# Performance work log

Hardware: AMD Instinct MI355X
Metric: run time of the kernel (lower is better)

Reference implementation:

```python
import jax, jax.numpy as jnp
import numpy as np

B, T, N, F, CH = 64, 8, 2000, 16, 64  # batch, timesteps(=receptive field), nodes, in features, channels (h_dim//2)
TASK = CH          # task_dim = h_dim // 2
P_TREAT = 0.5      # args.p
P1 = 1.0           # args.p1
BN_EPS = 1e-5


def setup_inputs() -> dict:
    key = jax.random.key(0)
    ks = jax.random.split(key, 40)
    def rn(i, shape, s=0.1):
        return jax.random.normal(ks[i], shape, dtype=jnp.float32) * s
    return {
        "X": jax.random.normal(ks[0], (B, T, N, F), dtype=jnp.float32),
        "A": jax.random.uniform(ks[1], (N, N), dtype=jnp.float32),
        "C": jax.random.randint(ks[2], (B, N), 0, 2, dtype=jnp.int32),
        "Y": jax.random.uniform(ks[3], (B, N), dtype=jnp.float32),
        "Cc": jnp.zeros((B, N), jnp.float32),
        "start_w": rn(4, (CH, F)),
        "start_b": rn(5, (CH,), 0.01),
        "filt_w": rn(6, (3, CH, CH, 2)),
        "filt_b": rn(7, (3, CH), 0.01),
        "gate_w": rn(8, (3, CH, CH, 2)),
        "gate_b": rn(9, (3, CH), 0.01),
        "skip_w": rn(10, (3, CH, CH)),
        "skip_b": rn(11, (3, CH), 0.01),
        "bn_g": 1.0 + rn(12, (3, CH), 0.01),
        "bn_b": rn(13, (3, CH), 0.01),
        "nodevec1": jax.random.normal(ks[14], (N, 10), dtype=jnp.float32),
        "nodevec2": jax.random.normal(ks[15], (10, N), dtype=jnp.float32),
        "task_emb": rn(16, (TASK,)),
        "gcn_w": rn(17, (CH, 3 * CH)),
        "gcn_b": rn(18, (CH,), 0.01),
        "h0_w1": rn(19, (CH, TASK + CH)),
        "h0_b1": rn(20, (CH,), 0.01),
        "h0_w2": rn(21, (1, CH)),
        "h0_b2": rn(22, (1,), 0.01),
        "h1_w1": rn(23, (CH, TASK + CH)),
        "h1_b1": rn(24, (CH,), 0.01),
        "h1_w2": rn(25, (1, CH)),
        "h1_b2": rn(26, (1,), 0.01),
    }


def _conv1x1(x, w, b):
    # x: (B,Cin,N,L), w: (Cout,Cin)
    return jnp.einsum('bcnl,oc->bonl', x, w) + b[None, :, None, None]


def _dil_conv(x, w, b, d):
    # kernel (1,2), dilation d along time, no padding -> width shrinks by d
    L = x.shape[-1]
    y = (jnp.einsum('bcnl,oc->bonl', x[..., :L - d], w[:, :, 0])
         + jnp.einsum('bcnl,oc->bonl', x[..., d:], w[:, :, 1]))
    return y + b[None, :, None, None]


def reference(X, A, C, Y, Cc, start_w, start_b, filt_w, filt_b, gate_w, gate_b,
              skip_w, skip_b, bn_g, bn_b, nodevec1, nodevec2, task_emb, gcn_w, gcn_b,
              h0_w1, h0_b1, h0_w2, h0_b2, h1_w1, h1_b1, h1_w2, h1_b2):
    x = jnp.transpose(X, (0, 3, 2, 1))            # (B,F,N,T)
    x = _conv1x1(x, start_w, start_b)             # (B,CH,N,T)
    adp = jax.nn.softmax(jax.nn.relu(nodevec1 @ nodevec2), axis=1)  # (N,N)
    skip = None
    d = 1
    for i in range(3):  # layers, dilations 1,2,4
        res = x
        f = jnp.tanh(_dil_conv(res, filt_w[i], filt_b[i], d))
        g = jax.nn.sigmoid(_dil_conv(res, gate_w[i], gate_b[i], d))
        x = f * g
        s = _conv1x1(x, skip_w[i], skip_b[i])
        skip = s if skip is None else s + skip[..., -s.shape[-1]:]
        x = x + res[..., -x.shape[-1]:]
        # eval-mode BatchNorm2d with running_mean=0, running_var=1
        scale = (bn_g[i] / jnp.sqrt(1.0 + BN_EPS))[None, :, None, None]
        x = x * scale + bn_b[i][None, :, None, None]
        d *= 2
    # gcn on skip (width 1): out = [x, A@x, A@(A@x)] -> concat -> 1x1 (dropout=eval identity)
    x1 = jnp.einsum('bcvl,vw->bcwl', skip, adp)
    x2 = jnp.einsum('bcvl,vw->bcwl', x1, adp)
    h = jnp.concatenate([skip, x1, x2], axis=1)   # (B,3CH,N,1)
    gx = jax.nn.relu(_conv1x1(h, gcn_w, gcn_b))   # (B,CH,N,1)
    bs, _, n_nodes, _ = gx.shape
    task = jnp.broadcast_to(task_emb[None, :, None, None], (bs, TASK, n_nodes, 1))
    z = jnp.concatenate([task, gx], axis=1)       # (B,TASK+CH,N,1)

    def hyp(w1, b1, w2, b2):
        hh = jax.nn.relu(_conv1x1(z, w1, b1))
        return _conv1x1(hh, w2, b2).reshape(-1)

    y1 = jax.nn.sigmoid(hyp(h1_w1, h1_b1, h1_w2, h1_b2))
    y0 = jax.nn.sigmoid(hyp(h0_w1, h0_b1, h0_w2, h0_b2))
    t = C.reshape(-1)
    y = jnp.where(t > 0, y1, y0)
    yc = jnp.clip(y, 1e-7, 1.0 - 1e-7)
    Yf = Y.reshape(-1)
    bce = -jnp.mean(Yf * jnp.log(yc) + (1.0 - Yf) * jnp.log(1.0 - yc))
    # linear MMD (mmd2_lin, CFR): masked means, jit-friendly
    zb = jnp.transpose(z, (0, 2, 1, 3)).reshape(bs * n_nodes, -1)  # (B*N, TASK+CH)
    tm = (t > 0).astype(zb.dtype)
    mean_t = (tm @ zb) / jnp.maximum(tm.sum(), 1.0)
    mean_c = ((1.0 - tm) @ zb) / jnp.maximum((1.0 - tm).sum(), 1.0)
    imb = jnp.sum((2.0 * P_TREAT * mean_t - 2.0 * (1.0 - P_TREAT) * mean_c) ** 2)
    loss = bce + P1 * imb
    return (loss, y, y0, y1)
```

## Files before the change

kernel.cpp:

```cpp
#include <hip/hip_runtime.h>
#include <cstdint>

#define NB 64
#define TT 8
#define NN 2000
#define NF 16
#define NCH 64
#define NPAD 2048
#define BCD 4096
#define ITEMS 128000

#define OFF_ADPF  0
#define OFF_ST    4194304
#define OFF_X2    0
#define OFF_ADPT  8388608
#define OFF_S     10485760
#define OFF_X1F   18874368
#define OFF_X1T   27262976
#define OFF_C01   31457280
#define OFF_WGCNT (OFF_C01 + 128)
#define OFF_W1TT  (OFF_WGCNT + 12288)
#define OFF_PART  (OFF_W1TT + 8192)
#define OFF_RED   (OFF_PART + 270336)
#define OFF_WAW   (OFF_RED + 136)
#define OFF_SWW   (OFF_WAW + 24576)
#define OFF_WSTW  (OFF_SWW + 6144)

#define SWZK(k, x) (((k) & ~63) | (((((k) >> 3) & 7) ^ ((x) & 7)) << 3) | ((k) & 7))
#define GSWZ(n) ((((n) >> 3) ^ (n)) & 7)

typedef __attribute__((ext_vector_type(8))) short short8;
typedef __attribute__((ext_vector_type(4))) float f32x4;
typedef const __attribute__((address_space(1))) uint32_t* gas_t;
typedef __attribute__((address_space(3))) uint32_t* las_t;

__device__ __forceinline__ float fast_rcp(float x) { return __builtin_amdgcn_rcpf(x); }
__device__ __forceinline__ float fast_tanh(float x) {
    x = fminf(fmaxf(x, -10.f), 10.f);
    float e = __expf(2.f * x);
    return (e - 1.f) * fast_rcp(e + 1.f);
}
__device__ __forceinline__ float fast_sigmoid(float x) {
    return fast_rcp(1.f + __expf(-x));
}
__device__ __forceinline__ unsigned short f2bf(float f) {
    uint32_t u = __float_as_uint(f);
    u += 0x7fff + ((u >> 16) & 1);
    return (unsigned short)(u >> 16);
}
__device__ __forceinline__ float bf2f(unsigned short b) {
    return __uint_as_float(((uint32_t)b) << 16);
}

__global__ __launch_bounds__(256) void prep_kernel(const float* __restrict__ gcn_w,
                            const float* __restrict__ h0_w1, const float* __restrict__ h0_b1,
                            const float* __restrict__ h1_w1, const float* __restrict__ h1_b1,
                            const float* __restrict__ task_emb,
                            const float* __restrict__ filt_w, const float* __restrict__ gate_w,
                            const float* __restrict__ skip_w, const float* __restrict__ start_w,
                            float* __restrict__ c01, float* __restrict__ wgcnT,
                            float* __restrict__ w1tT,
                            unsigned short* __restrict__ waw,
                            unsigned short* __restrict__ sww,
                            unsigned short* __restrict__ wstw)
{
    const int GS = 64 * 256;
    int gt = blockIdx.x * 256 + threadIdx.x;
    for (int idx = gt; idx < 64 * 192; idx += GS) {
        int o = idx / 192, j = idx % 192;
        wgcnT[j * 64 + o] = gcn_w[idx];
    }
    for (int idx = gt; idx < 4096; idx += GS) {
        int o = idx >> 6, c = idx & 63;
        w1tT[c * 64 + o]        = h0_w1[o * 128 + 64 + c];
        w1tT[4096 + c * 64 + o] = h1_w1[o * 128 + 64 + c];
    }
    for (int job = gt; job < 3 * 128 * 16; job += GS) {
        int L = job / 2048, rem = job % 2048;
        int r = rem >> 4, chp = rem & 15;
        int cho = chp ^ (r & 15);
        #pragma unroll
        for (int i = 0; i < 8; ++i) {
            int k = cho * 8 + i, tap = k >> 6, c = k & 63;
            float v = (r < 64) ? filt_w[L * 8192 + r * 128 + c * 2 + tap]
                               : gate_w[L * 8192 + (r - 64) * 128 + c * 2 + tap];
            waw[((L * 128 + r) * 16 + chp) * 8 + i] = f2bf(v);
        }
    }
    for (int job = gt; job < 3 * 64 * 8; job += GS) {
        int L = job / 512, rem = job % 512;
        int o = rem >> 3, chp = rem & 7;
        int cho = chp ^ (o & 7);
        #pragma unroll
        for (int i = 0; i < 8; ++i)
            sww[((L * 64 + o) * 8 + chp) * 8 + i] = f2bf(skip_w[L * 4096 + o * 64 + cho * 8 + i]);
    }
    for (int job = gt; job < 64 * 16; job += GS) {
        int o = job >> 4, chp = job & 15;
        int cho = chp ^ (o & 15);
        #pragma unroll
        for (int i = 0; i < 8; ++i) {
            int k = cho * 8 + i;
            wstw[(o * 16 + chp) * 8 + i] = (k < 16) ? f2bf(start_w[o * 16 + k]) : (unsigned short)0;
        }
    }
    if (gt < 128) {
        int head = gt >> 6, o = gt & 63;
        const float* w1 = head ? h1_w1 : h0_w1;
        const float* b1 = head ? h1_b1 : h0_b1;
        float a = b1[o];
        for (int k = 0; k < 64; ++k) a = fmaf(w1[o * 128 + k], task_emb[k], a);
        c01[gt] = a;
    }
}

__global__ __launch_bounds__(256) void adp_kernel(const float* __restrict__ nv1,
                                                  const float* __restrict__ nv2,
                                                  float* __restrict__ adpF)
{
    __shared__ float nv1s[10];
    __shared__ float rbuf[4];
    int tid = threadIdx.x;
    int r = blockIdx.x;
    if (tid < 10) nv1s[tid] = nv1[r * 10 + tid];
    __syncthreads();

    float val[8];
    float vmax = -3.4e38f;
    #pragma unroll
    for (int s = 0; s < 8; ++s) {
        int j = tid + s * 256;
        if (j < NN) {
            float v = 0.f;
            #pragma unroll
            for (int k = 0; k < 10; ++k) v = fmaf(nv1s[k], nv2[k * NN + j], v);
            v = fmaxf(v, 0.f);
            val[s] = v;
            vmax = fmaxf(vmax, v);
        } else val[s] = -3.4e38f;
    }
    for (int off = 32; off; off >>= 1) vmax = fmaxf(vmax, __shfl_down(vmax, off, 64));
    if ((tid & 63) == 0) rbuf[tid >> 6] = vmax;
    __syncthreads();
    vmax = fmaxf(fmaxf(rbuf[0], rbuf[1]), fmaxf(rbuf[2], rbuf[3]));
    __syncthreads();
    float sum = 0.f;
    #pragma unroll
    for (int s = 0; s < 8; ++s) {
        int j = tid + s * 256;
        if (j < NN) { val[s] = expf(val[s] - vmax); sum += val[s]; }
    }
    for (int off = 32; off; off >>= 1) sum += __shfl_down(sum, off, 64);
    if ((tid & 63) == 0) rbuf[tid >> 6] = sum;
    __syncthreads();
    sum = rbuf[0] + rbuf[1] + rbuf[2] + rbuf[3];
    float inv = 1.f / sum;
    #pragma unroll
    for (int s = 0; s < 8; ++s) {
        int j = tid + s * 256;
        if (j < NN) adpF[(size_t)r * NPAD + j] = val[s] * inv;
    }
}

__global__ __launch_bounds__(256) void transpose_adp(const float* __restrict__ adpF,
                                                     unsigned short* __restrict__ adpT)
{
    __shared__ float tile[64][65];
    int tid = threadIdx.x;
    int r0 = blockIdx.x * 64;
    int j0 = blockIdx.y * 64;
    #pragma unroll
    for (int s = 0; s < 16; ++s) {
        int idx = s * 256 + tid;
        int i = idx >> 6, jj = idx & 63;
        int r = r0 + i, j = j0 + jj;
        tile[i][jj] = (r < NN && j < NN) ? adpF[(size_t)r * NPAD + j] : 0.f;
    }
    __syncthreads();
    #pragma unroll
    for (int s = 0; s < 2; ++s) {
        int slot = s * 256 + tid;
        int j = slot >> 3, ch = slot & 7;
        short8 v;
        #pragma unroll
        for (int e = 0; e < 8; ++e) v[e] = (short)f2bf(tile[ch * 8 + e][j]);
        *(short8*)&adpT[(size_t)(j0 + j) * NPAD + r0 + ((ch ^ (j & 7)) << 3)] = v;
    }
}

template<int NG, int WOUT>
__device__ __forceinline__ void mfma_phaseB(int L,
    const unsigned short* __restrict__ xb, unsigned short* __restrict__ gbuf,
    const unsigned short* __restrict__ WA, const float* __restrict__ biasAll,
    int wave, int lr, int lk)
{
    if (wave >= NG) return;
    int idx = wave * 16 + lr;
    int n = (idx / WOUT) * 8 + (idx % WOUT);
    f32x4 aF[4], aG[4];
    #pragma unroll
    for (int mt = 0; mt < 4; ++mt) {
        aF[mt] = (f32x4){0.f, 0.f, 0.f, 0.f};
        aG[mt] = (f32x4){0.f, 0.f, 0.f, 0.f};
    }
    #pragma unroll
    for (int ks = 0; ks < 4; ++ks) {
        short8 bv = *(const short8*)&xb[(n * 16 + ((ks * 4 + lk) ^ (n & 15))) * 8];
        #pragma unroll
        for (int mt = 0; mt < 4; ++mt) {
            int r = mt * 16 + lr;
            short8 av = *(const short8*)&WA[(r * 16 + ((ks * 4 + lk) ^ (r & 15))) * 8];
            aF[mt] = __builtin_amdgcn_mfma_f32_16x16x32_bf16(av, bv, aF[mt], 0, 0, 0);
        }
        #pragma unroll
        for (int mt = 0; mt < 4; ++mt) {
            int r = (mt + 4) * 16 + lr;
            short8 av = *(const short8*)&WA[(r * 16 + ((ks * 4 + lk) ^ (r & 15))) * 8];
            aG[mt] = __builtin_amdgcn_mfma_f32_16x16x32_bf16(av, bv, aG[mt], 0, 0, 0);
        }
    }
    int gs = GSWZ(n);
    #pragma unroll
    for (int mt = 0; mt < 4; ++mt) {
        int ob = mt * 16 + lk * 4;
        ushort4 p;
        p.x = f2bf(fast_tanh(aF[mt][0] + biasAll[L * 128 + ob + 0]) * fast_sigmoid(aG[mt][0] + biasAll[L * 128 + 64 + ob + 0]));
        p.y = f2bf(fast_tanh(aF[mt][1] + biasAll[L * 128 + ob + 1]) * fast_sigmoid(aG[mt][1] + biasAll[L * 128 + 64 + ob + 1]));
        p.z = f2bf(fast_tanh(aF[mt][2] + biasAll[L * 128 + ob + 2]) * fast_sigmoid(aG[mt][2] + biasAll[L * 128 + 64 + ob + 2]));
        p.w = f2bf(fast_tanh(aF[mt][3] + biasAll[L * 128 + ob + 3]) * fast_sigmoid(aG[mt][3] + biasAll[L * 128 + 64 + ob + 3]));
        *(ushort4*)&gbuf[((n * 8) + ((mt * 2 + (lk >> 1)) ^ gs)) * 8 + (lk & 1) * 4] = p;
    }
}

template<int L, int D, int WOUT, int DN>
__device__ __forceinline__ void phaseC_conv(unsigned short* __restrict__ xb,
    const unsigned short* __restrict__ gbuf,
    const float* __restrict__ bn_g, const float* __restrict__ bn_b,
    float xreg[2][8], int wave, int o)
{
    const int WOUT_NEXT = WOUT - DN;
    float bsc = bn_g[L * 64 + o] * rsqrtf(1.0f + 1e-5f);
    float bsh = bn_b[L * 64 + o];
    #pragma unroll
    for (int gi = 0; gi < 2; ++gi) {
        int g = wave * 2 + gi;
        #pragma unroll
        for (int t = 0; t < WOUT; ++t) {
            int n = g * 8 + t;
            float gv = bf2f(gbuf[(n * 8 + ((o >> 3) ^ GSWZ(n))) * 8 + (o & 7)]);
            float nx = (gv + xreg[gi][t + D]) * bsc + bsh;
            xreg[gi][t] = nx;
            unsigned short bfv = f2bf(nx);
            if (t < WOUT_NEXT)
                xb[(n * 16 + ((o >> 3) ^ (n & 15))) * 8 + (o & 7)] = bfv;
            if (t >= DN) {
                int n1 = n - DN;
                xb[(n1 * 16 + (((o >> 3) + 8) ^ (n1 & 15))) * 8 + (o & 7)] = bfv;
            }
        }
    }
}

__device__ __forceinline__ void phaseC_skip(int L, int LASTT,
    const unsigned short* __restrict__ gbuf, const unsigned short* __restrict__ SW,
    f32x4 skacc[4], int wave, int lr, int lk)
{
    if (wave >= 2) return;
    int g = wave * 16 + lr;
    int n = g * 8 + LASTT;
    int gs = GSWZ(n);
    #pragma unroll
    for (int ks = 0; ks < 2; ++ks) {
        short8 bv = *(const short8*)&gbuf[(n * 8 + ((ks * 4 + lk) ^ gs)) * 8];
        #pragma unroll
        for (int mt = 0; mt < 4; ++mt) {
            int r = mt * 16 + lr;
            short8 av = *(const short8*)&SW[((L * 64 + r) * 8 + ((ks * 4 + lk) ^ (r & 7))) * 8];
            skacc[mt] = __builtin_amdgcn_mfma_f32_16x16x32_bf16(av, bv, skacc[mt], 0, 0, 0);
        }
    }
}

__global__ __launch_bounds__(1024) void temporal_kernel(
    const float* __restrict__ X,
    const float* __restrict__ start_b,
    const unsigned short* __restrict__ waw,
    const unsigned short* __restrict__ sww,
    const unsigned short* __restrict__ wstw,
    const float* __restrict__ filt_b, const float* __restrict__ gate_b,
    const float* __restrict__ skip_b,
    const float* __restrict__ bn_g, const float* __restrict__ bn_b,
    float* __restrict__ S, unsigned short* __restrict__ St)
{
    extern __shared__ float smem[];
    unsigned short* xb   = (unsigned short*)smem;
    unsigned short* gbuf = (unsigned short*)(smem + 16384);
    unsigned short* WA   = (unsigned short*)(smem + 24576);
    unsigned short* SW   = (unsigned short*)(smem + 32768);
    float* biasAll       = smem + 38912;

    int tid = threadIdx.x;
    int wave = tid >> 6, lane = tid & 63;
    int lr = lane & 15, lk = lane >> 4;
    int o = lane;
    int item0 = blockIdx.x * 32;

    __builtin_amdgcn_global_load_lds((gas_t)(wstw + tid * 8), (las_t)(WA + tid * 8), 16, 0, 0);
    for (int idx = tid; idx < 1536; idx += 1024)
        __builtin_amdgcn_global_load_lds((gas_t)(sww + idx * 8), (las_t)(SW + idx * 8), 16, 0, 0);
    if (tid < 384) {
        int L = tid >> 7, oo = tid & 127;
        biasAll[tid] = (oo < 64) ? filt_b[L * 64 + oo] : gate_b[L * 64 + oo - 64];
    }
    {
        int n = tid >> 2, c = tid & 3;
        int g = n >> 3, t = n & 7;
        int ig = item0 + g, b = ig / NN, nn = ig - b * NN;
        short8 v = {0, 0, 0, 0, 0, 0, 0, 0};
        if (c < 2) {
            const float* src = &X[((size_t)(b * TT + t) * NN + nn) * NF + c * 8];
            float4 f0 = *(const float4*)src;
            float4 f1 = *(const float4*)(src + 4);
            v[0] = (short)f2bf(f0.x); v[1] = (short)f2bf(f0.y);
            v[2] = (short)f2bf(f0.z); v[3] = (short)f2bf(f0.w);
            v[4] = (short)f2bf(f1.x); v[5] = (short)f2bf(f1.y);
            v[6] = (short)f2bf(f1.z); v[7] = (short)f2bf(f1.w);
        }
        *(short8*)&xb[(n * 16 + (c ^ (n & 15))) * 8] = v;
    }
    __syncthreads();

    {
        f32x4 aS[4];
        #pragma unroll
        for (int mt = 0; mt < 4; ++mt) aS[mt] = (f32x4){0.f, 0.f, 0.f, 0.f};
        int n = wave * 16 + lr;
        short8 bv = *(const short8*)&xb[(n * 16 + (lk ^ (n & 15))) * 8];
        #pragma unroll
        for (int mt = 0; mt < 4; ++mt) {
            int r = mt * 16 + lr;
            short8 av = *(const short8*)&WA[(r * 16 + (lk ^ (r & 15))) * 8];
            aS[mt] = __builtin_amdgcn_mfma_f32_16x16x32_bf16(av, bv, aS[mt], 0, 0, 0);
        }
        int gs = GSWZ(n);
        #pragma unroll
        for (int mt = 0; mt < 4; ++mt) {
            ushort4 p;
            p.x = f2bf(aS[mt][0]); p.y = f2bf(aS[mt][1]);
            p.z = f2bf(aS[mt][2]); p.w = f2bf(aS[mt][3]);
            *(ushort4*)&gbuf[((n * 8) + ((mt * 2 + (lk >> 1)) ^ gs)) * 8 + (lk & 1) * 4] = p;
        }
    }
    __syncthreads();

    float xreg[2][8];
    f32x4 skacc[4];
    #pragma unroll
    for (int mt = 0; mt < 4; ++mt) skacc[mt] = (f32x4){0.f, 0.f, 0.f, 0.f};

    {
        __builtin_amdgcn_global_load_lds((gas_t)(waw + (size_t)tid * 8),
                                         (las_t)(WA + tid * 8), 16, 0, 0);
        __builtin_amdgcn_global_load_lds((gas_t)(waw + (size_t)(tid + 1024) * 8),
                                         (las_t)(WA + (tid + 1024) * 8), 16, 0, 0);
        float sb = start_b[o];
        #pragma unroll
        for (int gi = 0; gi < 2; ++gi) {
            int g = wave * 2 + gi;
            #pragma unroll
            for (int t = 0; t < 8; ++t) {
                int n = g * 8 + t;
                float gv = bf2f(gbuf[(n * 8 + ((o >> 3) ^ GSWZ(n))) * 8 + (o & 7)]) + sb;
                xreg[gi][t] = gv;
                unsigned short bfv = f2bf(gv);
                if (t < 7)
                    xb[(n * 16 + ((o >> 3) ^ (n & 15))) * 8 + (o & 7)] = bfv;
                if (t >= 1) {
                    int n1 = n - 1;
                    xb[(n1 * 16 + (((o >> 3) + 8) ^ (n1 & 15))) * 8 + (o & 7)] = bfv;
                }
            }
        }
    }
    __syncthreads();

    mfma_phaseB<14, 7>(0, xb, gbuf, WA, biasAll, wave, lr, lk);
    __syncthreads();
    phaseC_skip(0, 6, gbuf, SW, skacc, wave, lr, lk);
    phaseC_conv<0, 1, 7, 2>(xb, gbuf, bn_g, bn_b, xreg, wave, o);
    __builtin_amdgcn_global_load_lds((gas_t)(waw + (size_t)(2048 + tid) * 8),
                                     (las_t)(WA + tid * 8), 16, 0, 0);
    __builtin_amdgcn_global_load_lds((gas_t)(waw + (size_t)(2048 + tid + 1024) * 8),
                                     (las_t)(WA + (tid + 1024) * 8), 16, 0, 0);
    __syncthreads();

    mfma_phaseB<10, 5>(1, xb, gbuf, WA, biasAll, wave, lr, lk);
    __syncthreads();
    phaseC_skip(1, 4, gbuf, SW, skacc, wave, lr, lk);
    phaseC_conv<1, 2, 5, 4>(xb, gbuf, bn_g, bn_b, xreg, wave, o);
    __builtin_amdgcn_global_load_lds((gas_t)(waw + (size_t)(4096 + tid) * 8),
                                     (las_t)(WA + tid * 8), 16, 0, 0);
    __builtin_amdgcn_global_load_lds((gas_t)(waw + (size_t)(4096 + tid + 1024) * 8),
                                     (las_t)(WA + (tid + 1024) * 8), 16, 0, 0);
    __syncthreads();

    mfma_phaseB<2, 1>(2, xb, gbuf, WA, biasAll, wave, lr, lk);
    __syncthreads();
    phaseC_skip(2, 0, gbuf, SW, skacc, wave, lr, lk);

    if (wave < 2) {
        int g = wave * 16 + lr;
        int ig = item0 + g, b = ig / NN, nn = ig - b * NN;
        #pragma unroll
        for (int mt = 0; mt < 4; ++mt) {
            #pragma unroll
            for (int j = 0; j < 4; ++j) {
                int oo = mt * 16 + lk * 4 + j;
                float v = skacc[mt][j] + skip_b[oo] + skip_b[64 + oo] + skip_b[128 + oo];
                int bc = b * 64 + oo;
                S[(size_t)nn * BCD + bc] = v;
                St[(size_t)bc * NPAD + SWZK(nn, oo)] = f2bf(v);
            }
        }
    }
}

__global__ __launch_bounds__(256) void gemm_mfma(
    const unsigned short* __restrict__ A, const unsigned short* __restrict__ B,
    float* __restrict__ Cf, unsigned short* __restrict__ Ct)
{
    __shared__ unsigned short As[128 * 64];
    __shared__ unsigned short Bs[128 * 64];
    int tid = threadIdx.x;
    int wave = tid >> 6, lane = tid & 63;
    int lk = lane >> 4, lr = lane & 15;
    int n0 = blockIdx.x * 128, m0 = blockIdx.y * 128;
    int wm = wave >> 1, wn = wave & 1;

    f32x4 acc[4][4];
    #pragma unroll
    for (int i = 0; i < 4; ++i)
        #pragma unroll
        for (int j = 0; j < 4; ++j)
            acc[i][j] = (f32x4){0.f, 0.f, 0.f, 0.f};

    for (int k0 = 0; k0 < NPAD; k0 += 64) {
        #pragma unroll
        for (int i = 0; i < 4; ++i) {
            int chunk = wave * 4 + i;
            int row = chunk * 8 + (lane >> 3);
            int koff = (lane & 7) * 8;
            __builtin_amdgcn_global_load_lds(
                (gas_t)(A + (size_t)(m0 + row) * NPAD + k0 + koff),
                (las_t)(&As[chunk * 512]), 16, 0, 0);
            __builtin_amdgcn_global_load_lds(
                (gas_t)(B + (size_t)(n0 + row) * NPAD + k0 + koff),
                (las_t)(&Bs[chunk * 512]), 16, 0, 0);
        }
        __syncthreads();
        #pragma unroll
        for (int s = 0; s < 2; ++s) {
            short8 av[4], bv[4];
            #pragma unroll
            for (int f = 0; f < 4; ++f) {
                int m = wm * 64 + f * 16 + lr;
                int ca = ((s * 4 + lk) ^ (m & 7));
                av[f] = *(const short8*)&As[m * 64 + ca * 8];
                int n = wn * 64 + f * 16 + lr;
                int cb = ((s * 4 + lk) ^ (n & 7));
                bv[f] = *(const short8*)&Bs[n * 64 + cb * 8];
            }
            #pragma unroll
            for (int fi = 0; fi < 4; ++fi)
                #pragma unroll
                for (int fj = 0; fj < 4; ++fj)
                    acc[fi][fj] = __builtin_amdgcn_mfma_f32_16x16x32_bf16(
                        av[fi], bv[fj], acc[fi][fj], 0, 0, 0);
        }
        __syncthreads();
    }

    #pragma unroll
    for (int fi = 0; fi < 4; ++fi) {
        #pragma unroll
        for (int fj = 0; fj < 4; ++fj) {
            int m = m0 + wm * 64 + fi * 16 + lk * 4;
            int n = n0 + wn * 64 + fj * 16 + lr;
            f32x4 v = acc[fi][fj];
            if (Cf) {
                Cf[(size_t)(m + 0) * BCD + n] = v[0];
                Cf[(size_t)(m + 1) * BCD + n] = v[1];
                Cf[(size_t)(m + 2) * BCD + n] = v[2];
                Cf[(size_t)(m + 3) * BCD + n] = v[3];
            }
            if (Ct) {
                ushort4 p;
                p.x = f2bf(v[0]); p.y = f2bf(v[1]);
                p.z = f2bf(v[2]); p.w = f2bf(v[3]);
                *(ushort4*)&Ct[(size_t)n * NPAD + SWZK(m, n)] = p;
            }
        }
    }
}

__global__ __launch_bounds__(256) void head_kernel(
    const float* __restrict__ S, const float* __restrict__ x1f,
    const float* __restrict__ x2,
    const float* __restrict__ wgcnT, const float* __restrict__ gcn_b,
    const float* __restrict__ c01, const float* __restrict__ w1tT,
    const float* __restrict__ h0_w2, const float* __restrict__ h0_b2,
    const float* __restrict__ h1_w2, const float* __restrict__ h1_b2,
    const int* __restrict__ Ct, const float* __restrict__ Yf,
    float* __restrict__ out, float* __restrict__ partials)
{
    __shared__ float hl[4][4][192];
    __shared__ float gxl[4][4][64];
    int tid = threadIdx.x;
    int wave = tid >> 6, o = tid & 63;
    int wid = blockIdx.x * 4 + wave;
    float w2a = h0_w2[o], w2b = h1_w2[o];
    float b20 = h0_b2[0], b21 = h1_b2[0];
    float cb = gcn_b[o], c0a = c01[o], c0b = c01[64 + o];

    float accT = 0.f, accC = 0.f, bce = 0.f, cT = 0.f, cC = 0.f;

    for (int base = wid * 4; base < ITEMS; base += 2048 * 4) {
        #pragma unroll
        for (int it = 0; it < 4; ++it) {
            int item = base + it;
            int b = item / NN, n = item - b * NN;
            int bc = b * 64 + o;
            hl[wave][it][o]       = S[(size_t)n * BCD + bc];
            hl[wave][it][64 + o]  = x1f[(size_t)n * BCD + bc];
            hl[wave][it][128 + o] = x2[(size_t)n * BCD + bc];
        }
        float a0 = cb, a1 = cb, a2 = cb, a3 = cb;
        for (int j = 0; j < 192; ++j) {
            float w = wgcnT[j * 64 + o];
            a0 = fmaf(w, hl[wave][0][j], a0);
            a1 = fmaf(w, hl[wave][1][j], a1);
            a2 = fmaf(w, hl[wave][2][j], a2);
            a3 = fmaf(w, hl[wave][3][j], a3);
        }
        float gxv[4] = {fmaxf(a0, 0.f), fmaxf(a1, 0.f), fmaxf(a2, 0.f), fmaxf(a3, 0.f)};
        #pragma unroll
        for (int it = 0; it < 4; ++it) gxl[wave][it][o] = gxv[it];

        float p0[4], p1[4];
        #pragma unroll
        for (int it = 0; it < 4; ++it) { p0[it] = c0a; p1[it] = c0b; }
        for (int c = 0; c < 64; ++c) {
            float w0 = w1tT[c * 64 + o];
            float w1 = w1tT[4096 + c * 64 + o];
            float g0 = gxl[wave][0][c], g1 = gxl[wave][1][c];
            float g2 = gxl[wave][2][c], g3 = gxl[wave][3][c];
            p0[0] = fmaf(w0, g0, p0[0]); p0[1] = fmaf(w0, g1, p0[1]);
            p0[2] = fmaf(w0, g2, p0[2]); p0[3] = fmaf(w0, g3, p0[3]);
            p1[0] = fmaf(w1, g0, p1[0]); p1[1] = fmaf(w1, g1, p1[1]);
            p1[2] = fmaf(w1, g2, p1[2]); p1[3] = fmaf(w1, g3, p1[3]);
        }
        #pragma unroll
        for (int it = 0; it < 4; ++it) {
            float r0 = w2a * fmaxf(p0[it], 0.f);
            float r1 = w2b * fmaxf(p1[it], 0.f);
            #pragma unroll
            for (int off = 32; off; off >>= 1) {
                r0 += __shfl_down(r0, off, 64);
                r1 += __shfl_down(r1, off, 64);
            }
            int item = base + it;
            int tt = Ct[item];
            if (o == 0) {
                float y0 = 1.f / (1.f + expf(-(r0 + b20)));
                float y1 = 1.f / (1.f + expf(-(r1 + b21)));
                float y = (tt > 0) ? y1 : y0;
                out[1 + item] = y;
                out[1 + ITEMS + item] = y0;
                out[1 + 2 * ITEMS + item] = y1;
                float yc = fminf(fmaxf(y, 1e-7f), 1.f - 1e-7f);
                float Yv = Yf[item];
                bce -= Yv * logf(yc) + (1.f - Yv) * logf(1.f - yc);
                if (tt > 0) cT += 1.f; else cC += 1.f;
            }
            if (tt > 0) accT += gxv[it]; else accC += gxv[it];
        }
    }
    partials[wid * 132 + o] = accT;
    partials[wid * 132 + 64 + o] = accC;
    if (o == 0) {
        partials[wid * 132 + 128] = bce;
        partials[wid * 132 + 129] = cT;
        partials[wid * 132 + 130] = cC;
    }
}

__global__ __launch_bounds__(256) void reduce_kernel(const float* __restrict__ partials,
                                                     float* __restrict__ red)
{
    __shared__ float rb[4];
    int slot = blockIdx.x;
    int tid = threadIdx.x;
    float s = 0.f;
    for (int w = tid; w < 2048; w += 256) s += partials[w * 132 + slot];
    #pragma unroll
    for (int off = 32; off; off >>= 1) s += __shfl_down(s, off, 64);
    if ((tid & 63) == 0) rb[tid >> 6] = s;
    __syncthreads();
    if (tid == 0) red[slot] = rb[0] + rb[1] + rb[2] + rb[3];
}

__global__ void final_kernel(const float* __restrict__ red,
                             const float* __restrict__ task_emb,
                             float* __restrict__ out)
{
    int tid = threadIdx.x;
    float cT = red[129], cC = red[130];
    float iT = 1.f / fmaxf(cT, 1.f), iC = 1.f / fmaxf(cC, 1.f);
    float d1 = task_emb[tid] * (cT * iT) - task_emb[tid] * (cC * iC);
    float d2 = red[tid] * iT - red[64 + tid] * iC;
    float p = d1 * d1 + d2 * d2;
    #pragma unroll
    for (int off = 32; off; off >>= 1) p += __shfl_down(p, off, 64);
    if (tid == 0) out[0] = red[128] * (1.f / (float)ITEMS) + p;
}

extern "C" void kernel_launch(void* const* d_in, const int* in_sizes, int n_in,
                              void* d_out, int out_size, void* d_ws, size_t ws_size,
                              hipStream_t stream)
{
    const float* X       = (const float*)d_in[0];
    const int*   Ct      = (const int*)d_in[2];
    const float* Yf      = (const float*)d_in[3];
    const float* start_w = (const float*)d_in[5];
    const float* start_b = (const float*)d_in[6];
    const float* filt_w  = (const float*)d_in[7];
    const float* filt_b  = (const float*)d_in[8];
    const float* gate_w  = (const float*)d_in[9];
    const float* gate_b  = (const float*)d_in[10];
    const float* skip_w  = (const float*)d_in[11];
    const float* skip_b  = (const float*)d_in[12];
    const float* bn_g    = (const float*)d_in[13];
    const float* bn_b    = (const float*)d_in[14];
    const float* nv1     = (const float*)d_in[15];
    const float* nv2     = (const float*)d_in[16];
    const float* task    = (const float*)d_in[17];
    const float* gcn_w   = (const float*)d_in[18];
    const float* gcn_b   = (const float*)d_in[19];
    const float* h0_w1   = (const float*)d_in[20];
    const float* h0_b1   = (const float*)d_in[21];
    const float* h0_w2   = (const float*)d_in[22];
    const float* h0_b2   = (const float*)d_in[23];
    const float* h1_w1   = (const float*)d_in[24];
    const float* h1_b1   = (const float*)d_in[25];
    const float* h1_w2   = (const float*)d_in[26];
    const float* h1_b2   = (const float*)d_in[27];

    float* ws    = (float*)d_ws;
    float* adpF  = ws + OFF_ADPF;
    unsigned short* St   = (unsigned short*)(ws + OFF_ST);
    float* x2    = ws + OFF_X2;
    unsigned short* adpT = (unsigned short*)(ws + OFF_ADPT);
    float* S     = ws + OFF_S;
    float* x1f   = ws + OFF_X1F;
    unsigned short* x1t  = (unsigned short*)(ws + OFF_X1T);
    float* c01   = ws + OFF_C01;
    float* wgcnT = ws + OFF_WGCNT;
    float* w1tT  = ws + OFF_W1TT;
    float* part  = ws + OFF_PART;
    float* red   = ws + OFF_RED;
    unsigned short* waw  = (unsigned short*)(ws + OFF_WAW);
    unsigned short* sww  = (unsigned short*)(ws + OFF_SWW);
    unsigned short* wstw = (unsigned short*)(ws + OFF_WSTW);
    float* outp  = (float*)d_out;

    hipMemsetAsync(St, 0, (size_t)BCD * NPAD * sizeof(unsigned short), stream);

    prep_kernel<<<64, 256, 0, stream>>>(gcn_w, h0_w1, h0_b1, h1_w1, h1_b1, task,
                                        filt_w, gate_w, skip_w, start_w,
                                        c01, wgcnT, w1tT, waw, sww, wstw);
    adp_kernel<<<NN, 256, 0, stream>>>(nv1, nv2, adpF);
    dim3 tg(NPAD / 64, NPAD / 64);
    transpose_adp<<<tg, 256, 0, stream>>>(adpF, adpT);

    const int K2_LDS = 39296 * 4;
    hipFuncSetAttribute(reinterpret_cast<const void*>(temporal_kernel),
                        hipFuncAttributeMaxDynamicSharedMemorySize, K2_LDS);
    temporal_kernel<<<ITEMS / 32, 1024, K2_LDS, stream>>>(
        X, start_b, waw, sww, wstw, filt_b, gate_b,
        skip_b, bn_g, bn_b, S, St);

    dim3 gg(BCD / 128, NPAD / 128);
    gemm_mfma<<<gg, 256, 0, stream>>>(adpT, St, x1f, x1t);
    gemm_mfma<<<gg, 256, 0, stream>>>(adpT, x1t, x2, nullptr);

    head_kernel<<<512, 256, 0, stream>>>(S, x1f, x2, wgcnT, gcn_b, c01, w1tT,
                                         h0_w2, h0_b2, h1_w2, h1_b2,
                                         Ct, Yf, outp, part);
    reduce_kernel<<<131, 256, 0, stream>>>(part, red);
    final_kernel<<<1, 64, 0, stream>>>(red, task, outp);
}
```

Baseline: 530.3 us.

## Split dilated conv taps into two K=64 MFMA passes, halve temporal block items

```diff
diff --git a/kernel.cpp b/kernel.cpp
--- a/kernel.cpp
+++ b/kernel.cpp
@@ -75,33 +75,34 @@
         w1tT[c * 64 + o]        = h0_w1[o * 128 + 64 + c];
         w1tT[4096 + c * 64 + o] = h1_w1[o * 128 + 64 + c];
     }
-    for (int job = gt; job < 3 * 128 * 16; job += GS) {
+    for (int job = gt; job < 3 * 2 * 128 * 8; job += GS) {
         int L = job / 2048, rem = job % 2048;
-        int r = rem >> 4, chp = rem & 15;
-        int cho = chp ^ (r & 15);
+        int p = rem >> 10, rem2 = rem & 1023;
+        int r = rem2 >> 3, chp = rem2 & 7;
+        int cho = chp ^ (r & 7);
         #pragma unroll
         for (int i = 0; i < 8; ++i) {
-            int k = cho * 8 + i, tap = k >> 6, c = k & 63;
-            float v = (r < 64) ? filt_w[L * 8192 + r * 128 + c * 2 + tap]
-                               : gate_w[L * 8192 + (r - 64) * 128 + c * 2 + tap];
-            waw[((L * 128 + r) * 16 + chp) * 8 + i] = f2bf(v);
+            int c = cho * 8 + i;
+            float v = (r < 64) ? filt_w[L * 8192 + r * 128 + c * 2 + p]
+                               : gate_w[L * 8192 + (r - 64) * 128 + c * 2 + p];
+            waw[((L * 2 + p) * 128 + r) * 64 + chp * 8 + i] = f2bf(v);
         }
     }
     for (int job = gt; job < 3 * 64 * 8; job += GS) {
         int L = job / 512, rem = job % 512;
-        int o = rem >> 3, chp = rem & 7;
-        int cho = chp ^ (o & 7);
+        int r = rem >> 3, chp = rem & 7;
+        int cho = chp ^ (r & 7);
         #pragma unroll
         for (int i = 0; i < 8; ++i)
-            sww[((L * 64 + o) * 8 + chp) * 8 + i] = f2bf(skip_w[L * 4096 + o * 64 + cho * 8 + i]);
-    }
-    for (int job = gt; job < 64 * 16; job += GS) {
-        int o = job >> 4, chp = job & 15;
-        int cho = chp ^ (o & 15);
+            sww[(L * 64 + r) * 64 + chp * 8 + i] = f2bf(skip_w[L * 4096 + r * 64 + cho * 8 + i]);
+    }
+    for (int job = gt; job < 64 * 8; job += GS) {
+        int r = job >> 3, chp = job & 7;
+        int cho = chp ^ (r & 7);
         #pragma unroll
         for (int i = 0; i < 8; ++i) {
             int k = cho * 8 + i;
-            wstw[(o * 16 + chp) * 8 + i] = (k < 16) ? f2bf(start_w[o * 16 + k]) : (unsigned short)0;
+            wstw[r * 64 + chp * 8 + i] = (k < 16) ? f2bf(start_w[r * 16 + k]) : (unsigned short)0;
         }
     }
     if (gt < 128) {
@@ -188,7 +189,7 @@
     }
 }
 
-template<int NG, int WOUT>
+template<int NG, int WOUT, int D>
 __device__ __forceinline__ void mfma_phaseB(int L,
     const unsigned short* __restrict__ xb, unsigned short* __restrict__ gbuf,
     const unsigned short* __restrict__ WA, const float* __restrict__ biasAll,
@@ -204,19 +205,24 @@
         aG[mt] = (f32x4){0.f, 0.f, 0.f, 0.f};
     }
     #pragma unroll
-    for (int ks = 0; ks < 4; ++ks) {
-        short8 bv = *(const short8*)&xb[(n * 16 + ((ks * 4 + lk) ^ (n & 15))) * 8];
-        #pragma unroll
-        for (int mt = 0; mt < 4; ++mt) {
-            int r = mt * 16 + lr;
-            short8 av = *(const short8*)&WA[(r * 16 + ((ks * 4 + lk) ^ (r & 15))) * 8];
-            aF[mt] = __builtin_amdgcn_mfma_f32_16x16x32_bf16(av, bv, aF[mt], 0, 0, 0);
-        }
-        #pragma unroll
-        for (int mt = 0; mt < 4; ++mt) {
-            int r = (mt + 4) * 16 + lr;
-            short8 av = *(const short8*)&WA[(r * 16 + ((ks * 4 + lk) ^ (r & 15))) * 8];
-            aG[mt] = __builtin_amdgcn_mfma_f32_16x16x32_bf16(av, bv, aG[mt], 0, 0, 0);
+    for (int p = 0; p < 2; ++p) {
+        int nb = n + p * D;
+        const unsigned short* WAp = WA + p * 8192;
+        #pragma unroll
+        for (int ks = 0; ks < 2; ++ks) {
+            short8 bv = *(const short8*)&xb[(nb * 8 + ((ks * 4 + lk) ^ (nb & 7))) * 8];
+            #pragma unroll
+            for (int mt = 0; mt < 4; ++mt) {
+                int r = mt * 16 + lr;
+                short8 av = *(const short8*)&WAp[(r * 8 + ((ks * 4 + lk) ^ (r & 7))) * 8];
+                aF[mt] = __builtin_amdgcn_mfma_f32_16x16x32_bf16(av, bv, aF[mt], 0, 0, 0);
+            }
+            #pragma unroll
+            for (int mt = 0; mt < 4; ++mt) {
+                int r = (mt + 4) * 16 + lr;
+                short8 av = *(const short8*)&WAp[(r * 8 + ((ks * 4 + lk) ^ (r & 7))) * 8];
+                aG[mt] = __builtin_amdgcn_mfma_f32_16x16x32_bf16(av, bv, aG[mt], 0, 0, 0);
+            }
         }
     }
     int gs = GSWZ(n);
@@ -232,42 +238,31 @@
     }
 }
 
-template<int L, int D, int WOUT, int DN>
+template<int L, int D, int WOUT>
 __device__ __forceinline__ void phaseC_conv(unsigned short* __restrict__ xb,
     const unsigned short* __restrict__ gbuf,
     const float* __restrict__ bn_g, const float* __restrict__ bn_b,
-    float xreg[2][8], int wave, int o)
-{
-    const int WOUT_NEXT = WOUT - DN;
+    float xreg[8], int wave, int o)
+{
     float bsc = bn_g[L * 64 + o] * rsqrtf(1.0f + 1e-5f);
     float bsh = bn_b[L * 64 + o];
-    #pragma unroll
-    for (int gi = 0; gi < 2; ++gi) {
-        int g = wave * 2 + gi;
-        #pragma unroll
-        for (int t = 0; t < WOUT; ++t) {
-            int n = g * 8 + t;
-            float gv = bf2f(gbuf[(n * 8 + ((o >> 3) ^ GSWZ(n))) * 8 + (o & 7)]);
-            float nx = (gv + xreg[gi][t + D]) * bsc + bsh;
-            xreg[gi][t] = nx;
-            unsigned short bfv = f2bf(nx);
-            if (t < WOUT_NEXT)
-                xb[(n * 16 + ((o >> 3) ^ (n & 15))) * 8 + (o & 7)] = bfv;
-            if (t >= DN) {
-                int n1 = n - DN;
-                xb[(n1 * 16 + (((o >> 3) + 8) ^ (n1 & 15))) * 8 + (o & 7)] = bfv;
-            }
-        }
-    }
-}
-
-__device__ __forceinline__ void phaseC_skip(int L, int LASTT,
+    int g = wave;
+    #pragma unroll
+    for (int t = 0; t < WOUT; ++t) {
+        int n = g * 8 + t;
+        float gv = bf2f(gbuf[(n * 8 + ((o >> 3) ^ GSWZ(n))) * 8 + (o & 7)]);
+        float nx = (gv + xreg[t + D]) * bsc + bsh;
+        xreg[t] = nx;
+        xb[(n * 8 + ((o >> 3) ^ (n & 7))) * 8 + (o & 7)] = f2bf(nx);
+    }
+}
+
+__device__ __forceinline__ void phaseC_skip(int LASTT,
     const unsigned short* __restrict__ gbuf, const unsigned short* __restrict__ SW,
     f32x4 skacc[4], int wave, int lr, int lk)
 {
-    if (wave >= 2) return;
-    int g = wave * 16 + lr;
-    int n = g * 8 + LASTT;
+    if (wave != 0) return;
+    int n = lr * 8 + LASTT;
     int gs = GSWZ(n);
     #pragma unroll
     for (int ks = 0; ks < 2; ++ks) {
@@ -275,7 +270,7 @@
         #pragma unroll
         for (int mt = 0; mt < 4; ++mt) {
             int r = mt * 16 + lr;
-            short8 av = *(const short8*)&SW[((L * 64 + r) * 8 + ((ks * 4 + lk) ^ (r & 7))) * 8];
+            short8 av = *(const short8*)&SW[(r * 8 + ((ks * 4 + lk) ^ (r & 7))) * 8];
             skacc[mt] = __builtin_amdgcn_mfma_f32_16x16x32_bf16(av, bv, skacc[mt], 0, 0, 0);
         }
     }
@@ -294,31 +289,31 @@
 {
     extern __shared__ float smem[];
     unsigned short* xb   = (unsigned short*)smem;
-    unsigned short* gbuf = (unsigned short*)(smem + 16384);
-    unsigned short* WA   = (unsigned short*)(smem + 24576);
-    unsigned short* SW   = (unsigned short*)(smem + 32768);
-    float* biasAll       = smem + 38912;
+    unsigned short* gbuf = (unsigned short*)(smem + 4096);
+    unsigned short* WA   = (unsigned short*)(smem + 8192);
+    unsigned short* SW   = (unsigned short*)(smem + 16384);
+    float* biasAll       = smem + 18432;
 
     int tid = threadIdx.x;
     int wave = tid >> 6, lane = tid & 63;
     int lr = lane & 15, lk = lane >> 4;
     int o = lane;
-    int item0 = blockIdx.x * 32;
-
-    __builtin_amdgcn_global_load_lds((gas_t)(wstw + tid * 8), (las_t)(WA + tid * 8), 16, 0, 0);
-    for (int idx = tid; idx < 1536; idx += 1024)
-        __builtin_amdgcn_global_load_lds((gas_t)(sww + idx * 8), (las_t)(SW + idx * 8), 16, 0, 0);
+    int item0 = blockIdx.x * 16;
+
+    if (tid < 512)
+        __builtin_amdgcn_global_load_lds((gas_t)(wstw + tid * 8), (las_t)(WA + tid * 8), 16, 0, 0);
     if (tid < 384) {
         int L = tid >> 7, oo = tid & 127;
         biasAll[tid] = (oo < 64) ? filt_b[L * 64 + oo] : gate_b[L * 64 + oo - 64];
     }
     {
-        int n = tid >> 2, c = tid & 3;
+        int n = tid >> 3, c = tid & 7;
         int g = n >> 3, t = n & 7;
         int ig = item0 + g, b = ig / NN, nn = ig - b * NN;
+        int cho = c ^ (n & 7);
         short8 v = {0, 0, 0, 0, 0, 0, 0, 0};
-        if (c < 2) {
-            const float* src = &X[((size_t)(b * TT + t) * NN + nn) * NF + c * 8];
+        if (cho < 2) {
+            const float* src = &X[((size_t)(b * TT + t) * NN + nn) * NF + cho * 8];
             float4 f0 = *(const float4*)src;
             float4 f1 = *(const float4*)(src + 4);
             v[0] = (short)f2bf(f0.x); v[1] = (short)f2bf(f0.y);
@@ -326,20 +321,20 @@
             v[4] = (short)f2bf(f1.x); v[5] = (short)f2bf(f1.y);
             v[6] = (short)f2bf(f1.z); v[7] = (short)f2bf(f1.w);
         }
-        *(short8*)&xb[(n * 16 + (c ^ (n & 15))) * 8] = v;
-    }
-    __syncthreads();
-
-    {
+        *(short8*)&xb[(n * 8 + c) * 8] = v;
+    }
+    __syncthreads();
+
+    if (wave < 8) {
         f32x4 aS[4];
         #pragma unroll
         for (int mt = 0; mt < 4; ++mt) aS[mt] = (f32x4){0.f, 0.f, 0.f, 0.f};
         int n = wave * 16 + lr;
-        short8 bv = *(const short8*)&xb[(n * 16 + (lk ^ (n & 15))) * 8];
+        short8 bv = *(const short8*)&xb[(n * 8 + (lk ^ (n & 7))) * 8];
         #pragma unroll
         for (int mt = 0; mt < 4; ++mt) {
             int r = mt * 16 + lr;
-            short8 av = *(const short8*)&WA[(r * 16 + (lk ^ (r & 15))) * 8];
+            short8 av = *(const short8*)&WA[(r * 8 + (lk ^ (r & 7))) * 8];
             aS[mt] = __builtin_amdgcn_mfma_f32_16x16x32_bf16(av, bv, aS[mt], 0, 0, 0);
         }
         int gs = GSWZ(n);
@@ -351,9 +346,11 @@
             *(ushort4*)&gbuf[((n * 8) + ((mt * 2 + (lk >> 1)) ^ gs)) * 8 + (lk & 1) * 4] = p;
         }
     }
-    __syncthreads();
-
-    float xreg[2][8];
+    if (tid < 512)
+        __builtin_amdgcn_global_load_lds((gas_t)(sww + tid * 8), (las_t)(SW + tid * 8), 16, 0, 0);
+    __syncthreads();
+
+    float xreg[8];
     f32x4 skacc[4];
     #pragma unroll
     for (int mt = 0; mt < 4; ++mt) skacc[mt] = (f32x4){0.f, 0.f, 0.f, 0.f};
@@ -364,53 +361,49 @@
         __builtin_amdgcn_global_load_lds((gas_t)(waw + (size_t)(tid + 1024) * 8),
                                          (las_t)(WA + (tid + 1024) * 8), 16, 0, 0);
         float sb = start_b[o];
-        #pragma unroll
-        for (int gi = 0; gi < 2; ++gi) {
-            int g = wave * 2 + gi;
-            #pragma unroll
-            for (int t = 0; t < 8; ++t) {
-                int n = g * 8 + t;
-                float gv = bf2f(gbuf[(n * 8 + ((o >> 3) ^ GSWZ(n))) * 8 + (o & 7)]) + sb;
-                xreg[gi][t] = gv;
-                unsigned short bfv = f2bf(gv);
-                if (t < 7)
-                    xb[(n * 16 + ((o >> 3) ^ (n & 15))) * 8 + (o & 7)] = bfv;
-                if (t >= 1) {
-                    int n1 = n - 1;
-                    xb[(n1 * 16 + (((o >> 3) + 8) ^ (n1 & 15))) * 8 + (o & 7)] = bfv;
-                }
-            }
-        }
-    }
-    __syncthreads();
-
-    mfma_phaseB<14, 7>(0, xb, gbuf, WA, biasAll, wave, lr, lk);
-    __syncthreads();
-    phaseC_skip(0, 6, gbuf, SW, skacc, wave, lr, lk);
-    phaseC_conv<0, 1, 7, 2>(xb, gbuf, bn_g, bn_b, xreg, wave, o);
-    __builtin_amdgcn_global_load_lds((gas_t)(waw + (size_t)(2048 + tid) * 8),
+        int g = wave;
+        #pragma unroll
+        for (int t = 0; t < 8; ++t) {
+            int n = g * 8 + t;
+            float gv = bf2f(gbuf[(n * 8 + ((o >> 3) ^ GSWZ(n))) * 8 + (o & 7)]) + sb;
+            xreg[t] = gv;
+            xb[(n * 8 + ((o >> 3) ^ (n & 7))) * 8 + (o & 7)] = f2bf(gv);
+        }
+    }
+    __syncthreads();
+
+    mfma_phaseB<7, 7, 1>(0, xb, gbuf, WA, biasAll, wave, lr, lk);
+    __syncthreads();
+    phaseC_skip(6, gbuf, SW, skacc, wave, lr, lk);
+    phaseC_conv<0, 1, 7>(xb, gbuf, bn_g, bn_b, xreg, wave, o);
+    __builtin_amdgcn_global_load_lds((gas_t)(waw + (size_t)(16384 + tid * 8)),
                                      (las_t)(WA + tid * 8), 16, 0, 0);
-    __builtin_amdgcn_global_load_lds((gas_t)(waw + (size_t)(2048 + tid + 1024) * 8),
+    __builtin_amdgcn_global_load_lds((gas_t)(waw + (size_t)(16384 + (tid + 1024) * 8)),
                                      (las_t)(WA + (tid + 1024) * 8), 16, 0, 0);
     __syncthreads();
 
-    mfma_phaseB<10, 5>(1, xb, gbuf, WA, biasAll, wave, lr, lk);
-    __syncthreads();
-    phaseC_skip(1, 4, gbuf, SW, skacc, wave, lr, lk);
-    phaseC_conv<1, 2, 5, 4>(xb, gbuf, bn_g, bn_b, xreg, wave, o);
-    __builtin_amdgcn_global_load_lds((gas_t)(waw + (size_t)(4096 + tid) * 8),
+    mfma_phaseB<5, 5, 2>(1, xb, gbuf, WA, biasAll, wave, lr, lk);
+    if (tid < 512)
+        __builtin_amdgcn_global_load_lds((gas_t)(sww + (size_t)(4096 + tid * 8)),
+                                         (las_t)(SW + tid * 8), 16, 0, 0);
+    __syncthreads();
+    phaseC_skip(4, gbuf, SW, skacc, wave, lr, lk);
+    phaseC_conv<1, 2, 5>(xb, gbuf, bn_g, bn_b, xreg, wave, o);
+    __builtin_amdgcn_global_load_lds((gas_t)(waw + (size_t)(32768 + tid * 8)),
                                      (las_t)(WA + tid * 8), 16, 0, 0);
-    __builtin_amdgcn_global_load_lds((gas_t)(waw + (size_t)(4096 + tid + 1024) * 8),
+    __builtin_amdgcn_global_load_lds((gas_t)(waw + (size_t)(32768 + (tid + 1024) * 8)),
                                      (las_t)(WA + (tid + 1024) * 8), 16, 0, 0);
     __syncthreads();
 
-    mfma_phaseB<2, 1>(2, xb, gbuf, WA, biasAll, wave, lr, lk);
-    __syncthreads();
-    phaseC_skip(2, 0, gbuf, SW, skacc, wave, lr, lk);
-
-    if (wave < 2) {
-        int g = wave * 16 + lr;
-        int ig = item0 + g, b = ig / NN, nn = ig - b * NN;
+    mfma_phaseB<1, 1, 4>(2, xb, gbuf, WA, biasAll, wave, lr, lk);
+    if (tid < 512)
+        __builtin_amdgcn_global_load_lds((gas_t)(sww + (size_t)(8192 + tid * 8)),
+                                         (las_t)(SW + tid * 8), 16, 0, 0);
+    __syncthreads();
+    phaseC_skip(0, gbuf, SW, skacc, wave, lr, lk);
+
+    if (wave == 0) {
+        int ig = item0 + lr, b = ig / NN, nn = ig - b * NN;
         #pragma unroll
         for (int mt = 0; mt < 4; ++mt) {
             #pragma unroll
@@ -682,10 +675,10 @@
     dim3 tg(NPAD / 64, NPAD / 64);
     transpose_adp<<<tg, 256, 0, stream>>>(adpF, adpT);
 
-    const int K2_LDS = 39296 * 4;
+    const int K2_LDS = 18816 * 4;
     hipFuncSetAttribute(reinterpret_cast<const void*>(temporal_kernel),
                         hipFuncAttributeMaxDynamicSharedMemorySize, K2_LDS);
-    temporal_kernel<<<ITEMS / 32, 1024, K2_LDS, stream>>>(
+    temporal_kernel<<<ITEMS / 16, 1024, K2_LDS, stream>>>(
         X, start_b, waw, sww, wstw, filt_b, gate_b,
         skip_b, bn_g, bn_b, S, St);
 
```

Measured after the change: 629.1 us. +18.6%, slower.
